# Kernel optimization log

Hardware: AMD Instinct MI355X
Metric: run time of the kernel (lower is better)

Reference implementation:

```python
import jax, jax.numpy as jnp
import numpy as np

B, S, E, D, H = 32, 4096, 512, 512, 512


def setup_inputs() -> dict:
    key = jax.random.key(0)
    ks = jax.random.split(key, 7)
    scale = 1.0 / np.sqrt(H)
    return {
        "encoder_hiddens": jax.random.normal(ks[0], (B, S, E), dtype=jnp.float32),
        "decoder_hidden": jax.random.normal(ks[1], (B, D), dtype=jnp.float32),
        "W_enc": jax.random.uniform(ks[2], (H, E), jnp.float32, -scale, scale),
        "b_enc": jax.random.uniform(ks[3], (H,), jnp.float32, -scale, scale),
        "W_dec": jax.random.uniform(ks[4], (H, D), jnp.float32, -scale, scale),
        "b_dec": jax.random.uniform(ks[5], (H,), jnp.float32, -scale, scale),
        "v": jax.random.uniform(ks[6], (H,), jnp.float32, -scale, scale),
    }


def reference(encoder_hiddens, decoder_hidden, W_enc, b_enc, W_dec, b_dec, v):
    # Projections (the two small GEMMs of the original per-timestep loop, batched)
    enc_hs = jnp.einsum("bse,he->bsh", encoder_hiddens, W_enc) + b_enc  # [B,S,H]
    dec_h = decoder_hidden @ W_dec.T + b_dec                            # [B,H]

    # Ragged-length detection: the torch loop breaks at the first all-zero
    # projected encoder row; positions at/after that are excluded (cumulative AND).
    nonzero = jnp.any(enc_hs != 0, axis=-1)                             # [B,S]
    valid = jnp.cumprod(nonzero.astype(jnp.int32), axis=1).astype(bool)

    # Additive (Bahdanau) scores: v . tanh(enc_hs + dec_h)
    scores = jnp.einsum("h,bsh->bs", v, jnp.tanh(enc_hs + dec_h[:, None, :]))
    scores = jnp.where(valid, scores, -jnp.inf)
    attn = jax.nn.softmax(scores, axis=1)                               # [B,S]
    attn = jnp.where(valid, attn, 0.0)

    # Weighted sum of encoder states -> context vector [B,1,E]
    return jnp.sum(encoder_hiddens * attn[..., None], axis=1, keepdims=True)
```

## Files before the change

### kernel.cpp

```cpp
#include <hip/hip_runtime.h>
#include <hip/hip_bf16.h>

#define BATCH 32
#define SEQ   4096
#define EDIM  512
#define HDIM  512
#define NCHUNK 64
#define NBLK  (BATCH * NCHUNK)

typedef unsigned short u16;
typedef unsigned int   u32;

typedef __bf16 bf16x8 __attribute__((ext_vector_type(8)));
typedef float  f32x4  __attribute__((ext_vector_type(4)));

__device__ __forceinline__ u32 cvtpk(float lo, float hi) {
    u32 r;
    asm("v_cvt_pk_bf16_f32 %0, %1, %2" : "=v"(r) : "v"(lo), "v"(hi));
    return r;
}
__device__ __forceinline__ float tanh_fast(float x) {
    float e = __builtin_amdgcn_exp2f(x * 2.88539008177793f);
    return 1.0f - 2.0f * __builtin_amdgcn_rcpf(e + 1.0f);
}

#define LDS_BARRIER() do {                                   \
    __builtin_amdgcn_sched_barrier(0);                       \
    asm volatile("s_waitcnt lgkmcnt(0)" ::: "memory");       \
    __builtin_amdgcn_s_barrier();                            \
    __builtin_amdgcn_sched_barrier(0);                       \
} while (0)

__global__ void prep_kernel(const float* __restrict__ W_enc, uint4* __restrict__ wpack,
                            const float* __restrict__ dec, const float* __restrict__ Wd,
                            const float* __restrict__ b_enc, const float* __restrict__ b_dec,
                            float* __restrict__ dec_bias) {
    int bid = blockIdx.x;
    int t = threadIdx.x;
    if (bid < 4096) {
        int wave = t >> 6, lane = t & 63;
        int p = bid * 4 + wave;
        int b = p >> 9, h = p & 511;
        const float4* wr = reinterpret_cast<const float4*>(Wd)  + h * 128;
        const float4* dr = reinterpret_cast<const float4*>(dec) + b * 128;
        float4 w0 = wr[lane * 2], w1 = wr[lane * 2 + 1];
        float4 d0 = dr[lane * 2], d1 = dr[lane * 2 + 1];
        float s = w0.x * d0.x + w0.y * d0.y + w0.z * d0.z + w0.w * d0.w
                + w1.x * d1.x + w1.y * d1.y + w1.z * d1.z + w1.w * d1.w;
#pragma unroll
        for (int m = 1; m < 64; m <<= 1) s += __shfl_xor(s, m, 64);
        if (lane == 0) dec_bias[p] = s + b_dec[h] + b_enc[h];
    } else {
        int id   = (bid - 4096) * 256 + t;
        int nsub = id >> 10;
        int rem  = id & 1023;
        int kc   = rem >> 6;
        int lane = rem & 63;
        int row  = nsub * 16 + (lane & 15);
        int col  = kc * 32 + (lane >> 4) * 8;
        const float* src = W_enc + row * EDIM + col;
        uint4 o;
        o.x = cvtpk(src[0], src[1]);
        o.y = cvtpk(src[2], src[3]);
        o.z = cvtpk(src[4], src[5]);
        o.w = cvtpk(src[6], src[7]);
        wpack[id] = o;
    }
}

#define ST 72

__global__ __launch_bounds__(512, 4) void fused_kernel(
    const float* __restrict__ X, const uint4* __restrict__ Wp,
    const float* __restrict__ bias, const float* __restrict__ v,
    float* __restrict__ cpart, float* __restrict__ mpart, float* __restrict__ lpart)
{
    __shared__ alignas(16) u16 Abuf[2][64 * ST];
    __shared__ float sred[8][64];
    __shared__ float pbuf[64];

    const int tid  = threadIdx.x;
    const int wave = tid >> 6, lane = tid & 63;
    const int quad = lane >> 4, l15 = lane & 15;
    const int blk  = blockIdx.x;
    const int b    = blk >> 6;
    const long row0 = (long)blk * 64;
    const float4* X4 = reinterpret_cast<const float4*>(X + row0 * EDIM);

    const int r  = tid >> 3;
    const int c8 = tid & 7;
    const float4* Xr = X4 + r * 128 + c8 * 2;
    u16* Aw0 = &Abuf[0][r * ST + c8 * 8];
    u16* Aw1 = &Abuf[1][r * ST + c8 * 8];

    float4 a0 = Xr[0], a1 = Xr[1];
    uint4 bA[4], bB[4];
#pragma unroll
    for (int jj = 0; jj < 4; jj++)
        bA[jj] = Wp[((wave * 4 + jj) * 16 + 0) * 64 + lane];
    float4 pA = Xr[16], pB = Xr[17];
    {
        uint4 w;
        w.x = cvtpk(a0.x, a0.y);  w.y = cvtpk(a0.z, a0.w);
        w.z = cvtpk(a1.x, a1.y);  w.w = cvtpk(a1.z, a1.w);
        *reinterpret_cast<uint4*>(Aw0) = w;
    }
    f32x4 acc[4][4] = {};
    LDS_BARRIER();

#pragma unroll
    for (int k = 0; k < 8; k++) {
        const u16* Ab = Abuf[k & 1];

#pragma unroll
        for (int jj = 0; jj < 4; jj++)
            bB[jj] = Wp[((wave * 4 + jj) * 16 + (2 * k + 1)) * 64 + lane];

        bf16x8 af[4];
#pragma unroll
        for (int i = 0; i < 4; i++)
            af[i] = *reinterpret_cast<const bf16x8*>(
                &Ab[(i * 16 + l15) * ST + quad * 8]);
#pragma unroll
        for (int jj = 0; jj < 4; jj++) {
            bf16x8 bfr = __builtin_bit_cast(bf16x8, bA[jj]);
#pragma unroll
            for (int i = 0; i < 4; i++)
                acc[i][jj] = __builtin_amdgcn_mfma_f32_16x16x32_bf16(
                    af[i], bfr, acc[i][jj], 0, 0, 0);
        }

        uint4 wq;
        if (k < 7) {
            wq.x = cvtpk(pA.x, pA.y);  wq.y = cvtpk(pA.z, pA.w);
            wq.z = cvtpk(pB.x, pB.y);  wq.w = cvtpk(pB.z, pB.w);
        }

        if (k < 7) {
#pragma unroll
            for (int jj = 0; jj < 4; jj++)
                bA[jj] = Wp[((wave * 4 + jj) * 16 + (2 * k + 2)) * 64 + lane];
        }

        if (k < 6) { pA = Xr[(k + 2) * 16]; pB = Xr[(k + 2) * 16 + 1]; }

#pragma unroll
        for (int i = 0; i < 4; i++)
            af[i] = *reinterpret_cast<const bf16x8*>(
                &Ab[(i * 16 + l15) * ST + 32 + quad * 8]);
#pragma unroll
        for (int jj = 0; jj < 4; jj++) {
            bf16x8 bfr = __builtin_bit_cast(bf16x8, bB[jj]);
#pragma unroll
            for (int i = 0; i < 4; i++)
                acc[i][jj] = __builtin_amdgcn_mfma_f32_16x16x32_bf16(
                    af[i], bfr, acc[i][jj], 0, 0, 0);
        }

        if (k < 7)
            *reinterpret_cast<uint4*>((k & 1) ? Aw0 : Aw1) = wq;

        if (k < 7) LDS_BARRIER();
    }

    float hb[4], hv[4];
#pragma unroll
    for (int jj = 0; jj < 4; jj++) {
        int h = wave * 64 + jj * 16 + l15;
        hb[jj] = bias[b * HDIM + h];
        hv[jj] = v[h];
    }
    float s_acc[16];
#pragma unroll
    for (int x = 0; x < 16; x++) s_acc[x] = 0.f;
#pragma unroll
    for (int i = 0; i < 4; i++)
#pragma unroll
        for (int jj = 0; jj < 4; jj++)
#pragma unroll
            for (int rr = 0; rr < 4; rr++)
                s_acc[i * 4 + rr] += hv[jj] * tanh_fast(acc[i][jj][rr] + hb[jj]);

#pragma unroll
    for (int m = 1; m < 16; m <<= 1)
#pragma unroll
        for (int x = 0; x < 16; x++)
            s_acc[x] += __shfl_xor(s_acc[x], m, 16);

    if (l15 == 0) {
#pragma unroll
        for (int x = 0; x < 16; x++) {
            int i = x >> 2, rr = x & 3;
            sred[wave][i * 16 + quad * 4 + rr] = s_acc[x];
        }
    }
    __syncthreads();

    if (tid < 64) {
        float sc = sred[0][tid] + sred[1][tid] + sred[2][tid] + sred[3][tid]
                 + sred[4][tid] + sred[5][tid] + sred[6][tid] + sred[7][tid];
        float mx = sc;
#pragma unroll
        for (int m = 1; m < 64; m <<= 1) mx = fmaxf(mx, __shfl_xor(mx, m, 64));
        float p = __builtin_amdgcn_exp2f((sc - mx) * 1.44269504088896f);
        float l = p;
#pragma unroll
        for (int m = 1; m < 64; m <<= 1) l += __shfl_xor(l, m, 64);
        pbuf[tid] = p;
        if (tid == 0) { mpart[blk] = mx; lpart[blk] = l; }
    }
    __syncthreads();

    const float* Xc = X + row0 * EDIM + tid;
    float a0c = 0.f, a1c = 0.f;
#pragma unroll 2
    for (int s = 0; s < 64; s += 8) {
        float x[8];
#pragma unroll
        for (int kk = 0; kk < 8; kk++) x[kk] = Xc[(s + kk) * EDIM];
#pragma unroll
        for (int kk = 0; kk < 8; kk += 2) {
            a0c = fmaf(pbuf[s + kk],     x[kk],     a0c);
            a1c = fmaf(pbuf[s + kk + 1], x[kk + 1], a1c);
        }
    }
    cpart[(long)blk * EDIM + tid] = a0c + a1c;
}

__global__ __launch_bounds__(256) void combine_k(const float* __restrict__ cpart,
                                                 const float* __restrict__ mpart,
                                                 const float* __restrict__ lpart,
                                                 float* __restrict__ out) {
    __shared__ float wbuf[64];
    __shared__ float linv_s;
    int b = blockIdx.x, t = threadIdx.x;
    if (t < 64) {
        float m = mpart[b * 64 + t];
        float M = m;
#pragma unroll
        for (int k = 1; k < 64; k <<= 1) M = fmaxf(M, __shfl_xor(M, k, 64));
        float w = __builtin_amdgcn_exp2f((m - M) * 1.44269504088896f);
        float lw = lpart[b * 64 + t] * w;
        float L = lw;
#pragma unroll
        for (int k = 1; k < 64; k <<= 1) L += __shfl_xor(L, k, 64);
        wbuf[t] = w;
        if (t == 0) linv_s = 1.0f / L;
    }
    __syncthreads();
    const float2* cp = reinterpret_cast<const float2*>(cpart) + (long)b * 64 * 256 + t;
    float ax = 0.f, ay = 0.f;
#pragma unroll 2
    for (int i = 0; i < 64; i += 8) {
        float2 x[8];
#pragma unroll
        for (int k = 0; k < 8; k++) x[k] = cp[(i + k) * 256];
#pragma unroll
        for (int k = 0; k < 8; k++) {
            float w = wbuf[i + k];
            ax = fmaf(w, x[k].x, ax);
            ay = fmaf(w, x[k].y, ay);
        }
    }
    float inv = linv_s;
    reinterpret_cast<float2*>(out)[b * 256 + t] = make_float2(ax * inv, ay * inv);
}

extern "C" void kernel_launch(void* const* d_in, const int* in_sizes, int n_in,
                              void* d_out, int out_size, void* d_ws, size_t ws_size,
                              hipStream_t stream) {
    const float* X      = (const float*)d_in[0];
    const float* dec    = (const float*)d_in[1];
    const float* W_enc  = (const float*)d_in[2];
    const float* b_enc  = (const float*)d_in[3];
    const float* W_dec  = (const float*)d_in[4];
    const float* b_dec  = (const float*)d_in[5];
    const float* v      = (const float*)d_in[6];
    float* out = (float*)d_out;

    char* ws = (char*)d_ws;
    uint4* wpack    = (uint4*)ws;
    float* dec_bias = (float*)(ws + (512 << 10));
    float* cpart    = (float*)(ws + (576 << 10));
    float* mpart    = (float*)(ws + (576 << 10) + (4096 << 10));
    float* lpart    = (float*)(ws + (576 << 10) + (4104 << 10));

    prep_kernel  <<<4224, 256, 0, stream>>>(W_enc, wpack, dec, W_dec, b_enc, b_dec,
                                            dec_bias);
    fused_kernel <<<NBLK, 512, 0, stream>>>(X, wpack, dec_bias, v, cpart, mpart, lpart);
    combine_k    <<<BATCH, 256, 0, stream>>>(cpart, mpart, lpart, out);
}
```

Before: 458.2 us.

## Split fused attention block across 16 waves with halved per-wave H tile

```diff
diff --git a/kernel.cpp b/kernel.cpp
--- a/kernel.cpp
+++ b/kernel.cpp
@@ -70,14 +70,60 @@
 
 #define ST 72
 
-__global__ __launch_bounds__(512, 4) void fused_kernel(
+#define KSTEP(k, Wc, Wn, pXc, pXn)                                              \
+    {                                                                           \
+        const u16* Ab_ = &Abuf[(k) & 1][0];                                     \
+        if ((k) < 7) {                                                          \
+            Wn[0] = Wq[(2 * (k) + 2) * 64];                                     \
+            Wn[1] = Wq[(16 + 2 * (k) + 2) * 64];                                \
+            Wn[2] = Wq[(2 * (k) + 3) * 64];                                     \
+            Wn[3] = Wq[(16 + 2 * (k) + 3) * 64];                                \
+        }                                                                       \
+        if ((k) < 6) pXn = Xr[((k) + 2) * 16];                                  \
+        bf16x8 af_[4];                                                          \
+        _Pragma("unroll")                                                       \
+        for (int i = 0; i < 4; i++)                                             \
+            af_[i] = *reinterpret_cast<const bf16x8*>(                          \
+                &Ab_[(i * 16 + l15) * ST + quad * 8]);                          \
+        _Pragma("unroll")                                                       \
+        for (int jj = 0; jj < 2; jj++) {                                        \
+            bf16x8 bfr = __builtin_bit_cast(bf16x8, Wc[jj]);                    \
+            _Pragma("unroll")                                                   \
+            for (int i = 0; i < 4; i++)                                         \
+                acc[i][jj] = __builtin_amdgcn_mfma_f32_16x16x32_bf16(           \
+                    af_[i], bfr, acc[i][jj], 0, 0, 0);                          \
+        }                                                                       \
+        if ((k) < 7) {                                                          \
+            uint2 wq_;                                                          \
+            wq_.x = cvtpk(pXc.x, pXc.y);                                        \
+            wq_.y = cvtpk(pXc.z, pXc.w);                                        \
+            *reinterpret_cast<uint2*>(                                          \
+                &Abuf[((k) + 1) & 1][r * ST + c4 * 4]) = wq_;                   \
+        }                                                                       \
+        _Pragma("unroll")                                                       \
+        for (int i = 0; i < 4; i++)                                             \
+            af_[i] = *reinterpret_cast<const bf16x8*>(                          \
+                &Ab_[(i * 16 + l15) * ST + 32 + quad * 8]);                     \
+        _Pragma("unroll")                                                       \
+        for (int jj = 0; jj < 2; jj++) {                                        \
+            bf16x8 bfr = __builtin_bit_cast(bf16x8, Wc[2 + jj]);                \
+            _Pragma("unroll")                                                   \
+            for (int i = 0; i < 4; i++)                                         \
+                acc[i][jj] = __builtin_amdgcn_mfma_f32_16x16x32_bf16(           \
+                    af_[i], bfr, acc[i][jj], 0, 0, 0);                          \
+        }                                                                       \
+        if ((k) < 7) LDS_BARRIER();                                             \
+    }
+
+__global__ __launch_bounds__(1024, 4) void fused_kernel(
     const float* __restrict__ X, const uint4* __restrict__ Wp,
     const float* __restrict__ bias, const float* __restrict__ v,
     float* __restrict__ cpart, float* __restrict__ mpart, float* __restrict__ lpart)
 {
     __shared__ alignas(16) u16 Abuf[2][64 * ST];
-    __shared__ float sred[8][64];
+    __shared__ float sred[16][64];
     __shared__ float pbuf[64];
+    __shared__ float cbuf[EDIM];
 
     const int tid  = threadIdx.x;
     const int wave = tid >> 6, lane = tid & 63;
@@ -87,86 +133,40 @@
     const long row0 = (long)blk * 64;
     const float4* X4 = reinterpret_cast<const float4*>(X + row0 * EDIM);
 
-    const int r  = tid >> 3;
-    const int c8 = tid & 7;
-    const float4* Xr = X4 + r * 128 + c8 * 2;
-    u16* Aw0 = &Abuf[0][r * ST + c8 * 8];
-    u16* Aw1 = &Abuf[1][r * ST + c8 * 8];
-
-    float4 a0 = Xr[0], a1 = Xr[1];
-    uint4 bA[4], bB[4];
-#pragma unroll
-    for (int jj = 0; jj < 4; jj++)
-        bA[jj] = Wp[((wave * 4 + jj) * 16 + 0) * 64 + lane];
-    float4 pA = Xr[16], pB = Xr[17];
+    const int r  = tid >> 4;
+    const int c4 = tid & 15;
+    const float4* Xr = X4 + r * 128 + c4;
+    const uint4* Wq = Wp + (wave * 2) * 16 * 64 + lane;
+
+    float4 x0 = Xr[0];
+    uint4 W0a[4], W1a[4];
+    W0a[0] = Wq[0];
+    W0a[1] = Wq[16 * 64];
+    W0a[2] = Wq[64];
+    W0a[3] = Wq[17 * 64];
+    float4 pX0 = Xr[16], pX1;
     {
-        uint4 w;
-        w.x = cvtpk(a0.x, a0.y);  w.y = cvtpk(a0.z, a0.w);
-        w.z = cvtpk(a1.x, a1.y);  w.w = cvtpk(a1.z, a1.w);
-        *reinterpret_cast<uint4*>(Aw0) = w;
-    }
-    f32x4 acc[4][4] = {};
+        uint2 w;
+        w.x = cvtpk(x0.x, x0.y);
+        w.y = cvtpk(x0.z, x0.w);
+        *reinterpret_cast<uint2*>(&Abuf[0][r * ST + c4 * 4]) = w;
+    }
+    f32x4 acc[4][2] = {};
     LDS_BARRIER();
 
-#pragma unroll
-    for (int k = 0; k < 8; k++) {
-        const u16* Ab = Abuf[k & 1];
-
-#pragma unroll
-        for (int jj = 0; jj < 4; jj++)
-            bB[jj] = Wp[((wave * 4 + jj) * 16 + (2 * k + 1)) * 64 + lane];
-
-        bf16x8 af[4];
-#pragma unroll
-        for (int i = 0; i < 4; i++)
-            af[i] = *reinterpret_cast<const bf16x8*>(
-                &Ab[(i * 16 + l15) * ST + quad * 8]);
-#pragma unroll
-        for (int jj = 0; jj < 4; jj++) {
-            bf16x8 bfr = __builtin_bit_cast(bf16x8, bA[jj]);
-#pragma unroll
-            for (int i = 0; i < 4; i++)
-                acc[i][jj] = __builtin_amdgcn_mfma_f32_16x16x32_bf16(
-                    af[i], bfr, acc[i][jj], 0, 0, 0);
-        }
-
-        uint4 wq;
-        if (k < 7) {
-            wq.x = cvtpk(pA.x, pA.y);  wq.y = cvtpk(pA.z, pA.w);
-            wq.z = cvtpk(pB.x, pB.y);  wq.w = cvtpk(pB.z, pB.w);
-        }
-
-        if (k < 7) {
-#pragma unroll
-            for (int jj = 0; jj < 4; jj++)
-                bA[jj] = Wp[((wave * 4 + jj) * 16 + (2 * k + 2)) * 64 + lane];
-        }
-
-        if (k < 6) { pA = Xr[(k + 2) * 16]; pB = Xr[(k + 2) * 16 + 1]; }
-
-#pragma unroll
-        for (int i = 0; i < 4; i++)
-            af[i] = *reinterpret_cast<const bf16x8*>(
-                &Ab[(i * 16 + l15) * ST + 32 + quad * 8]);
-#pragma unroll
-        for (int jj = 0; jj < 4; jj++) {
-            bf16x8 bfr = __builtin_bit_cast(bf16x8, bB[jj]);
-#pragma unroll
-            for (int i = 0; i < 4; i++)
-                acc[i][jj] = __builtin_amdgcn_mfma_f32_16x16x32_bf16(
-                    af[i], bfr, acc[i][jj], 0, 0, 0);
-        }
-
-        if (k < 7)
-            *reinterpret_cast<uint4*>((k & 1) ? Aw0 : Aw1) = wq;
-
-        if (k < 7) LDS_BARRIER();
-    }
-
-    float hb[4], hv[4];
-#pragma unroll
-    for (int jj = 0; jj < 4; jj++) {
-        int h = wave * 64 + jj * 16 + l15;
+    KSTEP(0, W0a, W1a, pX0, pX1)
+    KSTEP(1, W1a, W0a, pX1, pX0)
+    KSTEP(2, W0a, W1a, pX0, pX1)
+    KSTEP(3, W1a, W0a, pX1, pX0)
+    KSTEP(4, W0a, W1a, pX0, pX1)
+    KSTEP(5, W1a, W0a, pX1, pX0)
+    KSTEP(6, W0a, W1a, pX0, pX1)
+    KSTEP(7, W1a, W0a, pX1, pX0)
+
+    float hb[2], hv[2];
+#pragma unroll
+    for (int jj = 0; jj < 2; jj++) {
+        int h = wave * 32 + jj * 16 + l15;
         hb[jj] = bias[b * HDIM + h];
         hv[jj] = v[h];
     }
@@ -176,7 +176,7 @@
 #pragma unroll
     for (int i = 0; i < 4; i++)
 #pragma unroll
-        for (int jj = 0; jj < 4; jj++)
+        for (int jj = 0; jj < 2; jj++)
 #pragma unroll
             for (int rr = 0; rr < 4; rr++)
                 s_acc[i * 4 + rr] += hv[jj] * tanh_fast(acc[i][jj][rr] + hb[jj]);
@@ -197,8 +197,9 @@
     __syncthreads();
 
     if (tid < 64) {
-        float sc = sred[0][tid] + sred[1][tid] + sred[2][tid] + sred[3][tid]
-                 + sred[4][tid] + sred[5][tid] + sred[6][tid] + sred[7][tid];
+        float sc = 0.f;
+#pragma unroll
+        for (int w = 0; w < 16; w++) sc += sred[w][tid];
         float mx = sc;
 #pragma unroll
         for (int m = 1; m < 64; m <<= 1) mx = fmaxf(mx, __shfl_xor(mx, m, 64));
@@ -211,20 +212,27 @@
     }
     __syncthreads();
 
-    const float* Xc = X + row0 * EDIM + tid;
-    float a0c = 0.f, a1c = 0.f;
+    {
+        const int e    = tid & 511;
+        const int half = tid >> 9;
+        const float* Xc = X + row0 * EDIM + (long)(half * 32) * EDIM + e;
+        float a0 = 0.f, a1 = 0.f;
 #pragma unroll 2
-    for (int s = 0; s < 64; s += 8) {
-        float x[8];
-#pragma unroll
-        for (int kk = 0; kk < 8; kk++) x[kk] = Xc[(s + kk) * EDIM];
-#pragma unroll
-        for (int kk = 0; kk < 8; kk += 2) {
-            a0c = fmaf(pbuf[s + kk],     x[kk],     a0c);
-            a1c = fmaf(pbuf[s + kk + 1], x[kk + 1], a1c);
+        for (int s = 0; s < 32; s += 8) {
+            float x[8];
+#pragma unroll
+            for (int kk = 0; kk < 8; kk++) x[kk] = Xc[(s + kk) * EDIM];
+#pragma unroll
+            for (int kk = 0; kk < 8; kk += 2) {
+                a0 = fmaf(pbuf[half * 32 + s + kk],     x[kk],     a0);
+                a1 = fmaf(pbuf[half * 32 + s + kk + 1], x[kk + 1], a1);
+            }
         }
-    }
-    cpart[(long)blk * EDIM + tid] = a0c + a1c;
+        float tot = a0 + a1;
+        if (half) cbuf[e] = tot;
+        __syncthreads();
+        if (!half) cpart[(long)blk * EDIM + e] = tot + cbuf[e];
+    }
 }
 
 __global__ __launch_bounds__(256) void combine_k(const float* __restrict__ cpart,
@@ -287,6 +295,6 @@
 
     prep_kernel  <<<4224, 256, 0, stream>>>(W_enc, wpack, dec, W_dec, b_enc, b_dec,
                                             dec_bias);
-    fused_kernel <<<NBLK, 512, 0, stream>>>(X, wpack, dec_bias, v, cpart, mpart, lpart);
+    fused_kernel <<<NBLK, 1024, 0, stream>>>(X, wpack, dec_bias, v, cpart, mpart, lpart);
     combine_k    <<<BATCH, 256, 0, stream>>>(cpart, mpart, lpart, out);
 }
```

New measurement: 443.2 us. 3.3% less time.
